# Kernel optimization log

Measured on AMD Instinct MI355X. Metric: run time of the kernel, lower is better.

The kernel has to match this reference:

```python
import jax, jax.numpy as jnp
import numpy as np


def _gru_step(x, h, W_ih, W_hh, b_ih, b_hh):
    # torch GRUCell math, gate order (r, z, n)
    gx = x @ W_ih.T + b_ih
    gh = h @ W_hh.T + b_hh
    xr, xz, xn = jnp.split(gx, 3, axis=-1)
    hr, hz, hn = jnp.split(gh, 3, axis=-1)
    r = jax.nn.sigmoid(xr + hr)
    z = jax.nn.sigmoid(xz + hz)
    n = jnp.tanh(xn + r * hn)
    return (1.0 - z) * n + z * h


def setup_inputs() -> dict:
    T, B, S, E, H, Dv, EXT = 64, 16, 400, 128, 256, 50000, 50
    key = jax.random.key(0)
    ks = jax.random.split(key, 32)
    def rn(k, shape, s=0.05):
        return jax.random.normal(k, shape, dtype=jnp.float32) * s
    return {
        'embedded_y': rn(ks[0], (T, B, E), 1.0),
        'encode_outputs': rn(ks[1], (S, B, 2 * H), 1.0),
        'init_state': rn(ks[2], (B, H), 1.0),
        'x_mask': jnp.ones((S, B, 1), jnp.float32),
        'y_mask': jnp.ones((T, B, 1), jnp.float32),
        'x_index': jax.random.randint(ks[3], (S, B), 0, Dv + EXT),
        'max_ext_len': EXT,
        'init_coverage': jnp.zeros((B, S), jnp.float32),
        'W_h': rn(ks[4], (2 * H, 2 * H)),
        'W_s': rn(ks[5], (2 * H, H)),
        'W_c': rn(ks[6], (2 * H, 1)),
        'b_attn': rn(ks[7], (2 * H,)),
        'V_attn': rn(ks[8], (1, 2 * H)),
        'gru1_Wih': rn(ks[9], (3 * H, E)),
        'gru1_Whh': rn(ks[10], (3 * H, H)),
        'gru1_bih': rn(ks[11], (3 * H,)),
        'gru1_bhh': rn(ks[12], (3 * H,)),
        'gru2_Wih': rn(ks[13], (3 * H, 2 * H)),
        'gru2_Whh': rn(ks[14], (3 * H, H)),
        'gru2_bih': rn(ks[15], (3 * H,)),
        'gru2_bhh': rn(ks[16], (3 * H,)),
        'V1_w': rn(ks[17], (H, H + 2 * H + E)),
        'V1_b': rn(ks[18], (H,)),
        'V2_w': rn(ks[19], (Dv, H)),
        'V2_b': rn(ks[20], (Dv,)),
        'Wp_w': rn(ks[21], (1, H + 2 * H + E)),
        'Wp_b': rn(ks[22], (1,)),
    }


def reference(embedded_y, encode_outputs, init_state, x_mask, y_mask, x_index,
              max_ext_len, init_coverage, W_h, W_s, W_c, b_attn, V_attn,
              gru1_Wih, gru1_Whh, gru1_bih, gru1_bhh,
              gru2_Wih, gru2_Whh, gru2_bih, gru2_bhh,
              V1_w, V1_b, V2_w, V2_b, Wp_w, Wp_b):
    T, B, E = embedded_y.shape
    S = encode_outputs.shape[0]
    enc_proj = encode_outputs @ W_h.T  # [S,B,2H], time-invariant part of attention

    def step(carry, inp):
        hidden, cov = carry  # [B,H], [B,S]
        y_t, ym_t = inp      # [B,E], [B,1]
        s1 = _gru_step(y_t, hidden, gru1_Wih, gru1_Whh, gru1_bih, gru1_bhh)
        s1 = ym_t * s1 + (1.0 - ym_t) * hidden
        # coverage term: cov.T[:,:,None] is [S,B,1], Linear(1,2H)
        att = enc_proj + s1 @ W_s.T + cov.T[:, :, None] @ W_c.T + b_attn  # [S,B,2H]
        score = (jnp.tanh(att) * x_mask) @ V_attn.T                      # [S,B,1]
        score = jnp.where(x_mask == 0, -1e9, score)
        attn = jax.nn.softmax(score, axis=0)                             # over source len
        ctx = jnp.sum(attn * encode_outputs, axis=0)                     # [B,2H]
        s2 = _gru_step(ctx, s1, gru2_Wih, gru2_Whh, gru2_bih, gru2_bhh)
        s2 = ym_t * s2 + (1.0 - ym_t) * s1
        waw = attn[:, :, 0].T                                            # [B,S]
        return (s2, cov + waw), (s2, ctx, waw, cov)

    (_, _), (hs, cvs, waws, covs) = jax.lax.scan(
        step, (init_state, init_coverage), (embedded_y, y_mask))

    # WordProbLayer (pointer-generator)
    h = jnp.concatenate([hs, cvs, embedded_y], axis=2)         # [T,B,H+2H+E]
    logit = jnp.tanh(h @ V1_w.T + V1_b) @ V2_w.T + V2_b        # [T,B,Dv]
    y_dec = jax.nn.softmax(logit, axis=2)
    y_dec = jnp.concatenate(
        [y_dec, jnp.zeros((T, B, max_ext_len), y_dec.dtype)], axis=2)
    g = jax.nn.sigmoid(h @ Wp_w.T + Wp_b)                      # [T,B,1]
    xids = jnp.broadcast_to(x_index.T[None], (T, B, S))        # [T,B,S]
    ti = jnp.arange(T)[:, None, None]
    bi = jnp.arange(B)[None, :, None]
    y_pred = (g * y_dec).at[ti, bi, xids].add((1.0 - g) * waws)
    return (y_pred, hs, waws, covs)
```

## Files before the change

### kernel.cpp

```cpp
#include <hip/hip_runtime.h>
#include <hip/hip_bf16.h>

typedef unsigned short ushort_t;
typedef unsigned int u32;
typedef _Float16 f16;
typedef __attribute__((ext_vector_type(8))) short short8;
typedef __attribute__((ext_vector_type(4))) float f32x4;
typedef __attribute__((ext_vector_type(8))) _Float16 f16x8;
typedef __attribute__((ext_vector_type(4))) unsigned int u32x4;

#define T_ 64
#define B_ 16
#define S_ 400
#define E_ 128
#define H_ 256
#define H2_ 512
#define DV_ 50000
#define VOC_ 50050
#define CAT_ 896
#define NCLUS 8
#define RSL 50

#define YP_SZ   ((size_t)T_*B_*VOC_)
#define HS_OFF  (YP_SZ)
#define WW_OFF  (HS_OFF + (size_t)T_*B_*H_)
#define CV_OFF  (WW_OFF + (size_t)T_*B_*S_)
#define ENCP16_OFF ((size_t)0)
#define ENC16_OFF  ((size_t)1638400)
#define WS16_OFF   ((size_t)3276800)
#define W216_OFF   ((size_t)3342336)
#define CTXALL_OFF ((size_t)3538944)
#define GX1_OFF    ((size_t)4063232)
#define WH216_OFF  ((size_t)4947968)
#define WH116T_OFF ((size_t)5046272)
#define SYNC_OFF   ((size_t)5144576)
#define S1STR      528
#define S1TAG      520
#define S2STR      816
#define S2TAG      808
#define S2REG      ((size_t)16*NCLUS*S1STR)
#define SYNC_FLOATS ((size_t)16*NCLUS*(S1STR + S2STR))
#define WH16F_OFF  ((size_t)5316608)
#define V1HF_OFF   ((size_t)5447680)

#define WS_ROWSUM 0
#define WS_GV     1024
#define WS_G1     2048

__device__ __forceinline__ float fsig(float x){ return 1.f/(1.f+__expf(-x)); }
__device__ __forceinline__ float ftanh(float x){ float e=__expf(2.f*x); return 1.f - 2.f/(e+1.f); }

#define PADK(k) ((k) + (((k)>>5)<<2))

#define AT_ST(p, v)  __hip_atomic_store((p), (v), __ATOMIC_RELAXED, __HIP_MEMORY_SCOPE_AGENT)
#define AT_LD(p)     __hip_atomic_load((p), __ATOMIC_RELAXED, __HIP_MEMORY_SCOPE_AGENT)
#define AT_STI(p, v) __hip_atomic_store((int*)(p), (v), __ATOMIC_RELAXED, __HIP_MEMORY_SCOPE_AGENT)
#define AT_LDI(p)    __hip_atomic_load((const int*)(p), __ATOMIC_RELAXED, __HIP_MEMORY_SCOPE_AGENT)

#define SM_ENC    0
#define SM_ENCP   51200
#define SM_GH1    102400
#define SM_SWS    105472
#define SM_VP     107776
#define SM_WCP    110080
#define SM_UCTX   112384
#define SM_HID    114432
#define SM_S1     115456
#define SM_G2X    116480
#define SM_G2H    116864
#define SM_COV    117248
#define SM_EV     117504
#define SM_XM     117760
#define SM_YM     118016
#define SM_HIDH   118272
#define SM_S1H    118784
#define SM_CTXH   119296
#define SM_S2S    120320
#define SM_PART   120448
#define SM_B1     120512
#define SM_B2     123584
#define SM_B3     126656
#define SM_GX     129728
#define SM_BYTES  132800

__global__ __launch_bounds__(256)
void cvt16_kernel(const float* src, f16* dst, int n){
  int i = blockIdx.x*256 + threadIdx.x;
  if (i < n) dst[i] = (f16)src[i];
}

__global__ __launch_bounds__(256)
void repack_kernel(const float* enc, f16* enc16){
  int s = blockIdx.x, b = blockIdx.y;
  const float* src = enc + ((size_t)s*B_ + b)*H2_;
  f16* dst = enc16 + ((size_t)b*S_ + s)*H2_;
  for (int k = threadIdx.x; k < H2_; k += 256) dst[k] = (f16)src[k];
}

__global__ __launch_bounds__(256)
void packWhh1_kernel(const float* W, f16* dst){
  int r = blockIdx.x, c = threadIdx.x;
  int jq = c >> 5, cc = c & 31;
  dst[((size_t)jq*768 + r)*32 + cc] = (f16)W[(size_t)r*H_ + c];
}

__global__ __launch_bounds__(256)
void gx1_kernel(const float* emb, const float* Wih1, const float* bih1, float* dout){
  __shared__ float As[64][33];
  __shared__ float Bs[128][33];
  int m0 = blockIdx.x*64, n0 = blockIdx.y*128;
  int tx = threadIdx.x & 15, ty = threadIdx.x >> 4;
  float acc[4][8] = {};
  for (int kt = 0; kt < E_; kt += 32){
    for (int l = threadIdx.x; l < 64*32; l += 256){
      int m = l>>5, k = l&31; As[m][k] = emb[(size_t)(m0+m)*E_ + kt + k];
    }
    for (int l = threadIdx.x; l < 128*32; l += 256){
      int n = l>>5, k = l&31; Bs[n][k] = Wih1[(size_t)(n0+n)*E_ + kt + k];
    }
    __syncthreads();
    for (int k = 0; k < 32; ++k){
      float a[4], bv[8];
      #pragma unroll
      for (int i=0;i<4;++i) a[i] = As[ty+16*i][k];
      #pragma unroll
      for (int j=0;j<8;++j) bv[j] = Bs[tx+16*j][k];
      #pragma unroll
      for (int i=0;i<4;++i)
        #pragma unroll
        for (int j=0;j<8;++j) acc[i][j] += a[i]*bv[j];
    }
    __syncthreads();
  }
  #pragma unroll
  for (int i=0;i<4;++i)
    #pragma unroll
    for (int j=0;j<8;++j){
      int m = m0 + ty + 16*i, n = n0 + tx + 16*j;
      dout[GX1_OFF + (size_t)m*768 + n] = acc[i][j] + bih1[n];
    }
}

__global__ __launch_bounds__(256)
void encproj_mfma(const f16* enc16, const f16* Wh16, const float* battn, f16* ep16){
  int nx = blockIdx.x, my = blockIdx.y, bz = blockIdx.z;
  int tid = threadIdx.x;
  int w = tid >> 6, lane = tid & 63;
  int c16 = lane & 15, kg = lane >> 4;
  int m0 = my*64, n0 = nx*128 + w*32;
  f32x4 acc[4][2] = {};
  int col0 = n0 + c16, col1 = n0 + 16 + c16;
  for (int ks = 0; ks < 16; ++ks){
    int k0 = ks*32 + kg*8;
    f16x8 b0 = *(const f16x8*)(Wh16 + (size_t)col0*H2_ + k0);
    f16x8 b1 = *(const f16x8*)(Wh16 + (size_t)col1*H2_ + k0);
    #pragma unroll
    for (int mf = 0; mf < 4; ++mf){
      int s = m0 + mf*16 + c16; if (s > S_-1) s = S_-1;
      f16x8 a = *(const f16x8*)(enc16 + ((size_t)bz*S_ + s)*H2_ + k0);
      acc[mf][0] = __builtin_amdgcn_mfma_f32_16x16x32_f16(a, b0, acc[mf][0], 0, 0, 0);
      acc[mf][1] = __builtin_amdgcn_mfma_f32_16x16x32_f16(a, b1, acc[mf][1], 0, 0, 0);
    }
  }
  #pragma unroll
  for (int mf = 0; mf < 4; ++mf)
    #pragma unroll
    for (int nf = 0; nf < 2; ++nf){
      int col = n0 + nf*16 + c16;
      float bb = battn[col];
      #pragma unroll
      for (int r = 0; r < 4; ++r){
        int s = m0 + mf*16 + kg*4 + r;
        if (s < S_) ep16[((size_t)bz*S_ + s)*H2_ + col] = (f16)(acc[mf][nf][r] + bb);
      }
    }
}

template<int R, int K, bool PAD>
__device__ __forceinline__ void gemv_f16t(const f16* W, const f16* xh, float* out_l, int tid){
  int o = tid >> 3, l8 = tid & 7;
  constexpr int NI = K/64;
  const f16x8* x8 = (const f16x8*)xh;
  f16x8 xv[NI];
  #pragma unroll
  for (int i = 0; i < NI; ++i) xv[i] = x8[i*8 + l8];
  #pragma unroll
  for (int it = 0; it < R/128; ++it){
    int d = o + it*128;
    const f16x8* w8 = (const f16x8*)(W + (size_t)d*K);
    float acc = 0.f;
    #pragma unroll
    for (int i = 0; i < NI; ++i){
      f16x8 w = w8[i*8 + l8];
      #pragma unroll
      for (int e = 0; e < 8; ++e) acc += (float)w[e] * (float)xv[i][e];
    }
    acc += __shfl_xor(acc,1,8); acc += __shfl_xor(acc,2,8); acc += __shfl_xor(acc,4,8);
    if (l8 == 0) out_l[PAD ? PADK(d) : d] = acc;
  }
}

__device__ __forceinline__ void spin_tags(const float* base, int stride, int tagoff, int want, int tid){
  if (tid < 64){
    bool mine = tid < NCLUS;
    const float* tp = base + (size_t)(mine ? tid : 0)*stride + tagoff;
    while (true){
      int v = mine ? AT_LDI(tp) : want;
      if (__all(v == want)) break;
      __builtin_amdgcn_s_sleep(1);
    }
  }
  __syncthreads();
}

__global__ __launch_bounds__(1024)
void scan_kernel(const float* xm, const float* ym,
                 const float* bhh1, const float* bih2, const float* bhh2,
                 const float* Wc, const float* Vat,
                 const float* inith, const float* initc,
                 float* dout)
{
  extern __shared__ char smem[];
  f16*   enc_s  = (f16*)(smem + SM_ENC);
  f16*   encp_s = (f16*)(smem + SM_ENCP);
  float* gh1_l  = (float*)(smem + SM_GH1);
  float* sWs_p  = (float*)(smem + SM_SWS);
  float* Vp     = (float*)(smem + SM_VP);
  float* Wcp    = (float*)(smem + SM_WCP);
  float* uctx   = (float*)(smem + SM_UCTX);
  float* hid_l  = (float*)(smem + SM_HID);
  float* s1_l   = (float*)(smem + SM_S1);
  float* g2x_l  = (float*)(smem + SM_G2X);
  float* g2h_l  = (float*)(smem + SM_G2H);
  float* cov_l  = (float*)(smem + SM_COV);
  float* ev_l   = (float*)(smem + SM_EV);
  float* xm_l   = (float*)(smem + SM_XM);
  float* ym_l   = (float*)(smem + SM_YM);
  f16*   hidh   = (f16*)(smem + SM_HIDH);
  f16*   s1h    = (f16*)(smem + SM_S1H);
  f16*   ctxh   = (f16*)(smem + SM_CTXH);
  float* s2s    = (float*)(smem + SM_S2S);
  float* part_l = (float*)(smem + SM_PART);
  float* b1l    = (float*)(smem + SM_B1);
  float* b2l    = (float*)(smem + SM_B2);
  float* b3l    = (float*)(smem + SM_B3);
  float* gxbuf  = (float*)(smem + SM_GX);

  const f16* Ws16   = (const f16*)(dout + WS16_OFF);
  const f16* W216   = (const f16*)(dout + W216_OFF);
  const f16* Wh216  = (const f16*)(dout + WH216_OFF);
  const f16* Wh116T = (const f16*)(dout + WH116T_OFF);
  const float* gx1  = dout + GX1_OFF;

  int blk = blockIdx.x, tid = threadIdx.x;
  int b = blk & 15, jj = blk >> 4;
  int wv = tid >> 6, ln = tid & 63;

  float* sl1 = dout + SYNC_OFF + (size_t)b*NCLUS*S1STR;
  float* sl2 = dout + SYNC_OFF + S2REG + (size_t)b*NCLUS*S2STR;
  float* sl1my = sl1 + (size_t)jj*S1STR;
  float* sl2my = sl2 + (size_t)jj*S2STR;

  {
    const u32x4* encg  = (const u32x4*)(dout + ENC16_OFF)  + (size_t)b*25600 + jj*3200;
    const u32x4* encpg = (const u32x4*)(dout + ENCP16_OFF) + (size_t)b*25600 + jj*3200;
    u32x4* encs4  = (u32x4*)enc_s;
    u32x4* encps4 = (u32x4*)encp_s;
    for (int i = tid; i < 3200; i += 1024){ encs4[i] = encg[i]; encps4[i] = encpg[i]; }
  }
  if (tid < 32)  s2s[tid] = inith[b*H_ + jj*32 + tid];
  if (tid < 512){ Vp[PADK(tid)] = Vat[tid]; Wcp[PADK(tid)] = Wc[tid]; }
  if (tid < RSL){ int s = jj*RSL + tid; cov_l[tid] = initc[b*S_ + s]; xm_l[tid] = xm[(size_t)s*B_ + b]; }
  if (tid >= 512 && tid < 576) ym_l[tid-512] = ym[(tid-512)*B_ + b];
  if (tid < 768){ b1l[tid] = bhh1[tid]; b2l[tid] = bih2[tid]; b3l[tid] = bhh2[tid];
                  gxbuf[tid] = gx1[(size_t)b*768 + tid]; }
  __syncthreads();
  if (tid < 768){
    const f16x8* p8 = (const f16x8*)(Wh116T + ((size_t)jj*768 + tid)*32);
    float acc = 0.f;
    #pragma unroll
    for (int c4 = 0; c4 < 4; ++c4){
      f16x8 w = p8[c4];
      #pragma unroll
      for (int e = 0; e < 8; ++e) acc += (float)w[e] * s2s[c4*8+e];
    }
    AT_ST(&sl2my[tid], acc);
  } else if (tid < 800){
    AT_ST(&sl2my[768 + (tid-768)], s2s[tid-768]);
  }
  __syncthreads();
  if (tid == 0) AT_STI(&sl2my[S2TAG], 1);

  for (int t = 0; t < T_; ++t){
    int row = t*B_ + b;
    int want = t + 1;
    spin_tags(sl2, S2STR, S2TAG, want, tid);
    if (tid < 768){
      float a = 0.f;
      #pragma unroll
      for (int q = 0; q < NCLUS; ++q) a += AT_LD(&sl2[(size_t)q*S2STR + tid]);
      gh1_l[tid] = a;
    } else {
      int j = tid - 768;
      float h = AT_LD(&sl2[(size_t)(j>>5)*S2STR + 768 + (j&31)]);
      hid_l[j] = h; hidh[j] = (f16)h;
    }
    __syncthreads();
    if (tid < 256){
      int j = tid;
      float r = fsig(gxbuf[j]      + gh1_l[j]      + b1l[j]);
      float z = fsig(gxbuf[256+j]  + gh1_l[256+j]  + b1l[256+j]);
      float n = ftanh(gxbuf[512+j] + r*(gh1_l[512+j] + b1l[512+j]));
      float h = hid_l[j];
      float ymv = ym_l[t];
      float s1 = ymv*((1.f-z)*n + z*h) + (1.f-ymv)*h;
      s1_l[j] = s1; s1h[j] = (f16)s1;
    }
    __syncthreads();
    gemv_f16t<512,256,true>(Ws16, s1h, sWs_p, tid);
    __syncthreads();
    {
      int kp = PADK(ln*8);
      float4 sA = *(const float4*)&sWs_p[kp], sB = *(const float4*)&sWs_p[kp+4];
      float4 vA = *(const float4*)&Vp[kp],    vB = *(const float4*)&Vp[kp+4];
      float4 cA = *(const float4*)&Wcp[kp],   cB = *(const float4*)&Wcp[kp+4];
      const f16x8* eps = (const f16x8*)encp_s;
      #pragma unroll
      for (int i = 0; i < 4; ++i){
        int r = wv + 16*i;
        if (r < RSL){
          f16x8 eu = eps[r*64 + ln];
          float cv = cov_l[r];
          float sc = 0.f;
          sc += ftanh((float)eu[0] + sA.x + cv*cA.x)*vA.x;
          sc += ftanh((float)eu[1] + sA.y + cv*cA.y)*vA.y;
          sc += ftanh((float)eu[2] + sA.z + cv*cA.z)*vA.z;
          sc += ftanh((float)eu[3] + sA.w + cv*cA.w)*vA.w;
          sc += ftanh((float)eu[4] + sB.x + cv*cB.x)*vB.x;
          sc += ftanh((float)eu[5] + sB.y + cv*cB.y)*vB.y;
          sc += ftanh((float)eu[6] + sB.z + cv*cB.z)*vB.z;
          sc += ftanh((float)eu[7] + sB.w + cv*cB.w)*vB.w;
          sc += __shfl_xor(sc,1);  sc += __shfl_xor(sc,2);  sc += __shfl_xor(sc,4);
          sc += __shfl_xor(sc,8);  sc += __shfl_xor(sc,16); sc += __shfl_xor(sc,32);
          if (ln == 0){
            float xmv = xm_l[r];
            ev_l[r] = __expf((xmv == 0.f) ? -1e9f : xmv*sc);
          }
        }
      }
    }
    __syncthreads();
    if (tid < 512){
      float acc = 0.f;
      #pragma unroll 5
      for (int s = 0; s < RSL; ++s) acc += ev_l[s] * (float)enc_s[s*H2_ + tid];
      AT_ST(&sl1my[tid], acc);
    } else if (tid >= 960){
      int l = tid - 960;
      float v = (l < RSL) ? ev_l[l] : 0.f;
      v += __shfl_xor(v,1);  v += __shfl_xor(v,2);  v += __shfl_xor(v,4);
      v += __shfl_xor(v,8);  v += __shfl_xor(v,16); v += __shfl_xor(v,32);
      if (l == 0) AT_ST(&sl1my[512], v);
    }
    __syncthreads();
    if (tid == 0) AT_STI(&sl1my[S1TAG], want);
    float gxn = 0.f;
    if (tid < 768){
      int tn = (t+1 < T_) ? t+1 : t;
      gxn = gx1[(size_t)(tn*B_ + b)*768 + tid];
    }
    {
      int o = tid >> 3, l8 = tid & 7;
      if (o < 96){
        int g = o >> 5, m = o & 31, wrow = g*256 + jj*32 + m;
        const f16x8* w8 = (const f16x8*)(Wh216 + (size_t)wrow*H_);
        const f16x8* x8 = (const f16x8*)s1h;
        float acc = 0.f;
        #pragma unroll
        for (int i = 0; i < 4; ++i){
          f16x8 w = w8[i*8 + l8], x = x8[i*8 + l8];
          #pragma unroll
          for (int e = 0; e < 8; ++e) acc += (float)w[e] * (float)x[e];
        }
        acc += __shfl_xor(acc,1,8); acc += __shfl_xor(acc,2,8); acc += __shfl_xor(acc,4,8);
        if (l8 == 0) g2h_l[o] = acc;
      }
    }
    if (tid < 768) gxbuf[tid] = gxn;
    spin_tags(sl1, S1STR, S1TAG, want, tid);
    if (tid < 512){
      float us = 0.f;
      #pragma unroll
      for (int q = 0; q < NCLUS; ++q) us += AT_LD(&sl1[(size_t)q*S1STR + tid]);
      uctx[tid] = us;
    } else if (tid < 512 + NCLUS){
      part_l[tid-512] = AT_LD(&sl1[(size_t)(tid-512)*S1STR + 512]);
    }
    __syncthreads();
    {
      float es = 0.f;
      #pragma unroll
      for (int q = 0; q < NCLUS; ++q) es += part_l[q];
      float inv = 1.f/es;
      if (tid < 512){
        float v = uctx[tid]*inv;
        ctxh[tid] = (f16)v;
        if (jj == 0) __builtin_nontemporal_store(v, &dout[CTXALL_OFF + (size_t)row*H2_ + tid]);
      } else if (tid >= 640 && tid < 640 + RSL){
        int r = tid - 640;
        float w_ = ev_l[r]*inv;
        size_t ro = (size_t)row*S_ + jj*RSL + r;
        __builtin_nontemporal_store(w_, &dout[WW_OFF + ro]);
        float co = cov_l[r];
        __builtin_nontemporal_store(co, &dout[CV_OFF + ro]);
        cov_l[r] = co + w_;
      }
    }
    __syncthreads();
    {
      int o = tid >> 3, l8 = tid & 7;
      if (o < 96){
        int g = o >> 5, m = o & 31, wrow = g*256 + jj*32 + m;
        const f16x8* w8 = (const f16x8*)(W216 + (size_t)wrow*H2_);
        const f16x8* x8 = (const f16x8*)ctxh;
        float acc = 0.f;
        #pragma unroll
        for (int i = 0; i < 8; ++i){
          f16x8 w = w8[i*8 + l8], x = x8[i*8 + l8];
          #pragma unroll
          for (int e = 0; e < 8; ++e) acc += (float)w[e] * (float)x[e];
        }
        acc += __shfl_xor(acc,1,8); acc += __shfl_xor(acc,2,8); acc += __shfl_xor(acc,4,8);
        if (l8 == 0) g2x_l[o] = acc;
      }
    }
    __syncthreads();
    if (tid < 32){
      int i = tid, j = jj*32 + i;
      float r = fsig(g2x_l[i]     + b2l[j]     + g2h_l[i]    + b3l[j]);
      float z = fsig(g2x_l[32+i]  + b2l[256+j] + g2h_l[32+i] + b3l[256+j]);
      float n = ftanh(g2x_l[64+i] + b2l[512+j] + r*(g2h_l[64+i] + b3l[512+j]));
      float s1v = s1_l[j];
      float ymv = ym_l[t];
      float s2 = ymv*((1.f-z)*n + z*s1v) + (1.f-ymv)*s1v;
      s2s[i] = s2;
      AT_ST(&sl2my[768 + i], s2);
      __builtin_nontemporal_store(s2, &dout[HS_OFF + (size_t)row*H_ + j]);
    }
    __syncthreads();
    if (tid < 768){
      const f16x8* p8 = (const f16x8*)(Wh116T + ((size_t)jj*768 + tid)*32);
      float acc = 0.f;
      #pragma unroll
      for (int c4 = 0; c4 < 4; ++c4){
        f16x8 w = p8[c4];
        #pragma unroll
        for (int e = 0; e < 8; ++e) acc += (float)w[e] * s2s[c4*8+e];
      }
      AT_ST(&sl2my[tid], acc);
    }
    __syncthreads();
    if (tid == 0) AT_STI(&sl2my[S2TAG], t + 2);
  }
}

__global__ __launch_bounds__(512)
void head_kernel(const float* emb, const f16* V1H, const float* V1b,
                 const float* Wpw, const float* Wpb, float* dout, float* ws)
{
  __shared__ float hc[2][CAT_];
  int t = blockIdx.x, b0 = blockIdx.y*2, tid = threadIdx.x;
  for (int i = tid; i < 2*CAT_; i += 512){
    int bb = i / CAT_, k = i % CAT_;
    int b = b0 + bb;
    float v;
    if (k < H_)           v = dout[HS_OFF     + ((size_t)(t*B_+b))*H_  + k];
    else if (k < H_+H2_)  v = dout[CTXALL_OFF + ((size_t)(t*B_+b))*H2_ + (k-H_)];
    else                  v = emb[((size_t)(t*B_+b))*E_ + (k-H_-H2_)];
    hc[bb][k] = v;
  }
  __syncthreads();
  __hip_bfloat16* G1 = (__hip_bfloat16*)(ws + WS_G1);
  {
    int j = tid & 255, bb = tid >> 8;
    const f16x8* wv8 = (const f16x8*)(V1H + (size_t)j*CAT_);
    float acc = 0.f;
    #pragma unroll 4
    for (int kk = 0; kk < CAT_/8; ++kk){
      f16x8 w = wv8[kk];
      #pragma unroll
      for (int e = 0; e < 8; ++e) acc += hc[bb][kk*8+e]*(float)w[e];
    }
    G1[((size_t)(t*B_ + b0 + bb))*H_ + j] = __float2bfloat16(ftanh(acc + V1b[j]));
  }
  if (tid < 128){
    int bb = tid >> 6, l = tid & 63;
    float acc = 0.f;
    for (int k = l; k < CAT_; k += 64) acc += hc[bb][k]*Wpw[k];
    acc += __shfl_xor(acc,1);  acc += __shfl_xor(acc,2);  acc += __shfl_xor(acc,4);
    acc += __shfl_xor(acc,8);  acc += __shfl_xor(acc,16); acc += __shfl_xor(acc,32);
    if (l == 0) ws[WS_GV + t*B_ + b0 + bb] = fsig(acc + Wpb[0]);
  }
}

__global__ __launch_bounds__(256)
void gemm2_kernel(const ushort_t* G1, const float* V2w, const float* V2b,
                  float* dout, float* rowsum)
{
  __shared__ float rows_l[128];
  int tid = threadIdx.x;
  if (tid < 128) rows_l[tid] = 0.f;
  int m0 = blockIdx.y * 128;
  int n0 = blockIdx.x * 64;
  int lane = tid & 63, w = tid >> 6;
  int c16 = lane & 15, kg = lane >> 4;
  int col = n0 + w*16 + c16;
  int colc = col < DV_ ? col : DV_-1;
  bool valid = col < DV_;
  f32x4 acc[8] = {};
  const float* brow = V2w + (size_t)colc*H_;
  for (int ks = 0; ks < 8; ++ks){
    int k0 = ks*32 + kg*8;
    short8 bf;
    #pragma unroll
    for (int i = 0; i < 8; ++i){
      __hip_bfloat16 hb = __float2bfloat16(brow[k0+i]);
      union { __hip_bfloat16 h; short s; } u; u.h = hb;
      bf[i] = u.s;
    }
    #pragma unroll
    for (int mf = 0; mf < 8; ++mf){
      const short8* ap = (const short8*)(G1 + ((size_t)(m0 + mf*16 + c16))*H_ + k0);
      acc[mf] = __builtin_amdgcn_mfma_f32_16x16x32_bf16(*ap, bf, acc[mf], 0, 0, 0);
    }
  }
  float bias = valid ? V2b[colc] : 0.f;
  __syncthreads();
  #pragma unroll
  for (int mf = 0; mf < 8; ++mf){
    #pragma unroll
    for (int r = 0; r < 4; ++r){
      float v = valid ? __expf(acc[mf][r] + bias) : 0.f;
      int rloc = mf*16 + kg*4 + r;
      if (valid) dout[(size_t)(m0 + rloc)*VOC_ + col] = v;
      float s = v;
      s += __shfl_xor(s, 1, 16); s += __shfl_xor(s, 2, 16);
      s += __shfl_xor(s, 4, 16); s += __shfl_xor(s, 8, 16);
      if (c16 == 0) atomicAdd(&rows_l[rloc], s);
    }
  }
  __syncthreads();
  if (tid < 128) atomicAdd(&rowsum[m0 + tid], rows_l[tid]);
}

__global__ __launch_bounds__(256)
void normscatter_kernel(float* dout, const float* ws, const int* xidx){
  int row = blockIdx.x; int b = row & 15;
  float gv = ws[WS_GV + row];
  float sc = gv / ws[WS_ROWSUM + row];
  float g1 = 1.f - gv;
  float2* y2 = (float2*)(dout + (size_t)row * VOC_);
  for (int i = threadIdx.x; i < VOC_/2; i += 256){
    float2 v = y2[i];
    int e0 = 2*i;
    v.x = (e0   < DV_) ? v.x*sc : 0.f;
    v.y = (e0+1 < DV_) ? v.y*sc : 0.f;
    y2[i] = v;
  }
  __syncthreads();
  const float* ww = dout + WW_OFF + (size_t)row*S_;
  float* y = dout + (size_t)row*VOC_;
  for (int s = threadIdx.x; s < S_; s += 256){
    atomicAdd(&y[xidx[(size_t)s*B_ + b]], g1*ww[s]);
  }
}

extern "C" void kernel_launch(void* const* d_in, const int* in_sizes, int n_in,
                              void* d_out, int out_size, void* d_ws, size_t ws_size,
                              hipStream_t stream)
{
  (void)in_sizes; (void)n_in; (void)out_size; (void)ws_size;
  const float* emb   = (const float*)d_in[0];
  const float* enc   = (const float*)d_in[1];
  const float* inith = (const float*)d_in[2];
  const float* xmask = (const float*)d_in[3];
  const float* ymask = (const float*)d_in[4];
  const int*   xidx  = (const int*)d_in[5];
  const float* initc = (const float*)d_in[7];
  const float* Wh    = (const float*)d_in[8];
  const float* Wss   = (const float*)d_in[9];
  const float* Wc    = (const float*)d_in[10];
  const float* battn = (const float*)d_in[11];
  const float* Vat   = (const float*)d_in[12];
  const float* Wih1  = (const float*)d_in[13];
  const float* Whh1  = (const float*)d_in[14];
  const float* bih1  = (const float*)d_in[15];
  const float* bhh1  = (const float*)d_in[16];
  const float* Wih2  = (const float*)d_in[17];
  const float* Whh2  = (const float*)d_in[18];
  const float* bih2  = (const float*)d_in[19];
  const float* bhh2  = (const float*)d_in[20];
  const float* V1w   = (const float*)d_in[21];
  const float* V1b   = (const float*)d_in[22];
  const float* V2w   = (const float*)d_in[23];
  const float* V2b   = (const float*)d_in[24];
  const float* Wpw   = (const float*)d_in[25];
  const float* Wpb   = (const float*)d_in[26];
  float* out = (float*)d_out;
  float* ws  = (float*)d_ws;

  hipFuncSetAttribute(reinterpret_cast<const void*>(scan_kernel),
                      hipFuncAttributeMaxDynamicSharedMemorySize, SM_BYTES);

  hipMemsetAsync(d_ws, 0, 2048*sizeof(float), stream);
  hipMemsetAsync(out + SYNC_OFF, 0, SYNC_FLOATS*sizeof(float), stream);
  cvt16_kernel<<<512,  256, 0, stream>>>(Wss,  (f16*)(out + WS16_OFF), H2_*H_);
  cvt16_kernel<<<1536, 256, 0, stream>>>(Wih2, (f16*)(out + W216_OFF), 3*H_*H2_);
  cvt16_kernel<<<768,  256, 0, stream>>>(Whh2, (f16*)(out + WH216_OFF), 3*H_*H_);
  cvt16_kernel<<<1024, 256, 0, stream>>>(Wh,   (f16*)(out + WH16F_OFF), H2_*H2_);
  cvt16_kernel<<<896,  256, 0, stream>>>(V1w,  (f16*)(out + V1HF_OFF), H_*CAT_);
  packWhh1_kernel<<<768, 256, 0, stream>>>(Whh1, (f16*)(out + WH116T_OFF));
  repack_kernel<<<dim3(S_, B_), 256, 0, stream>>>(enc, (f16*)(out + ENC16_OFF));
  gx1_kernel<<<dim3(16, 6), 256, 0, stream>>>(emb, Wih1, bih1, out);
  encproj_mfma<<<dim3(4, 7, B_), 256, 0, stream>>>((const f16*)(out + ENC16_OFF),
      (const f16*)(out + WH16F_OFF), battn, (f16*)(out + ENCP16_OFF));
  scan_kernel<<<128, 1024, SM_BYTES, stream>>>(xmask, ymask,
      bhh1, bih2, bhh2, Wc, Vat, inith, initc, out);
  head_kernel<<<dim3(T_, 8), 512, 0, stream>>>(emb, (const f16*)(out + V1HF_OFF),
      V1b, Wpw, Wpb, out, ws);
  gemm2_kernel<<<dim3(782, 8), 256, 0, stream>>>((const ushort_t*)(ws + WS_G1), V2w, V2b, out, ws + WS_ROWSUM);
  normscatter_kernel<<<1024, 256, 0, stream>>>(out, ws, xidx);
}
```

Measured before the change: 1.888 ms.

## Remove scan-step barriers by fusing reductions and doubling gemm2 row tile

```diff
diff --git a/kernel.cpp b/kernel.cpp
--- a/kernel.cpp
+++ b/kernel.cpp
@@ -63,20 +63,15 @@
 #define SM_SWS    105472
 #define SM_VP     107776
 #define SM_WCP    110080
-#define SM_UCTX   112384
-#define SM_HID    114432
 #define SM_S1     115456
-#define SM_G2X    116480
 #define SM_G2H    116864
 #define SM_COV    117248
 #define SM_EV     117504
 #define SM_XM     117760
 #define SM_YM     118016
-#define SM_HIDH   118272
 #define SM_S1H    118784
 #define SM_CTXH   119296
 #define SM_S2S    120320
-#define SM_PART   120448
 #define SM_B1     120512
 #define SM_B2     123584
 #define SM_B3     126656
@@ -223,24 +218,18 @@
   extern __shared__ char smem[];
   f16*   enc_s  = (f16*)(smem + SM_ENC);
   f16*   encp_s = (f16*)(smem + SM_ENCP);
-  float* gh1_l  = (float*)(smem + SM_GH1);
   float* sWs_p  = (float*)(smem + SM_SWS);
   float* Vp     = (float*)(smem + SM_VP);
   float* Wcp    = (float*)(smem + SM_WCP);
-  float* uctx   = (float*)(smem + SM_UCTX);
-  float* hid_l  = (float*)(smem + SM_HID);
   float* s1_l   = (float*)(smem + SM_S1);
-  float* g2x_l  = (float*)(smem + SM_G2X);
   float* g2h_l  = (float*)(smem + SM_G2H);
   float* cov_l  = (float*)(smem + SM_COV);
   float* ev_l   = (float*)(smem + SM_EV);
   float* xm_l   = (float*)(smem + SM_XM);
   float* ym_l   = (float*)(smem + SM_YM);
-  f16*   hidh   = (f16*)(smem + SM_HIDH);
   f16*   s1h    = (f16*)(smem + SM_S1H);
   f16*   ctxh   = (f16*)(smem + SM_CTXH);
   float* s2s    = (float*)(smem + SM_S2S);
-  float* part_l = (float*)(smem + SM_PART);
   float* b1l    = (float*)(smem + SM_B1);
   float* b2l    = (float*)(smem + SM_B2);
   float* b3l    = (float*)(smem + SM_B3);
@@ -295,23 +284,18 @@
     int row = t*B_ + b;
     int want = t + 1;
     spin_tags(sl2, S2STR, S2TAG, want, tid);
-    if (tid < 768){
-      float a = 0.f;
-      #pragma unroll
-      for (int q = 0; q < NCLUS; ++q) a += AT_LD(&sl2[(size_t)q*S2STR + tid]);
-      gh1_l[tid] = a;
-    } else {
-      int j = tid - 768;
-      float h = AT_LD(&sl2[(size_t)(j>>5)*S2STR + 768 + (j&31)]);
-      hid_l[j] = h; hidh[j] = (f16)h;
-    }
-    __syncthreads();
     if (tid < 256){
       int j = tid;
-      float r = fsig(gxbuf[j]      + gh1_l[j]      + b1l[j]);
-      float z = fsig(gxbuf[256+j]  + gh1_l[256+j]  + b1l[256+j]);
-      float n = ftanh(gxbuf[512+j] + r*(gh1_l[512+j] + b1l[512+j]));
-      float h = hid_l[j];
+      float ar = 0.f, az = 0.f, an = 0.f;
+      #pragma unroll
+      for (int q = 0; q < NCLUS; ++q){
+        const float* sq = sl2 + (size_t)q*S2STR;
+        ar += AT_LD(&sq[j]); az += AT_LD(&sq[256+j]); an += AT_LD(&sq[512+j]);
+      }
+      float h = AT_LD(&sl2[(size_t)(j>>5)*S2STR + 768 + (j&31)]);
+      float r = fsig(gxbuf[j]      + ar + b1l[j]);
+      float z = fsig(gxbuf[256+j]  + az + b1l[256+j]);
+      float n = ftanh(gxbuf[512+j] + r*(an + b1l[512+j]));
       float ymv = ym_l[t];
       float s1 = ymv*((1.f-z)*n + z*h) + (1.f-ymv)*h;
       s1_l[j] = s1; s1h[j] = (f16)s1;
@@ -371,39 +355,43 @@
     }
     {
       int o = tid >> 3, l8 = tid & 7;
-      if (o < 96){
-        int g = o >> 5, m = o & 31, wrow = g*256 + jj*32 + m;
-        const f16x8* w8 = (const f16x8*)(Wh216 + (size_t)wrow*H_);
-        const f16x8* x8 = (const f16x8*)s1h;
-        float acc = 0.f;
+      if (o < 32){
+        int j = jj*32 + o;
+        const f16x8* y8 = (const f16x8*)s1h;
+        f16x8 ya[4];
+        #pragma unroll
+        for (int i = 0; i < 4; ++i) ya[i] = y8[i*8 + l8];
+        float ar = 0.f, az = 0.f, an = 0.f;
+        const f16x8* wr = (const f16x8*)(Wh216 + (size_t)j*H_);
+        const f16x8* wz = (const f16x8*)(Wh216 + (size_t)(256+j)*H_);
+        const f16x8* wn = (const f16x8*)(Wh216 + (size_t)(512+j)*H_);
         #pragma unroll
         for (int i = 0; i < 4; ++i){
-          f16x8 w = w8[i*8 + l8], x = x8[i*8 + l8];
+          f16x8 a = wr[i*8 + l8], c = wz[i*8 + l8], d = wn[i*8 + l8];
           #pragma unroll
-          for (int e = 0; e < 8; ++e) acc += (float)w[e] * (float)x[e];
+          for (int e = 0; e < 8; ++e){
+            float xv = (float)ya[i][e];
+            ar += (float)a[e]*xv; az += (float)c[e]*xv; an += (float)d[e]*xv;
+          }
         }
-        acc += __shfl_xor(acc,1,8); acc += __shfl_xor(acc,2,8); acc += __shfl_xor(acc,4,8);
-        if (l8 == 0) g2h_l[o] = acc;
+        ar += __shfl_xor(ar,1,8); ar += __shfl_xor(ar,2,8); ar += __shfl_xor(ar,4,8);
+        az += __shfl_xor(az,1,8); az += __shfl_xor(az,2,8); az += __shfl_xor(az,4,8);
+        an += __shfl_xor(an,1,8); an += __shfl_xor(an,2,8); an += __shfl_xor(an,4,8);
+        if (l8 == 0){ g2h_l[o] = ar; g2h_l[32+o] = az; g2h_l[64+o] = an; }
       }
     }
     if (tid < 768) gxbuf[tid] = gxn;
     spin_tags(sl1, S1STR, S1TAG, want, tid);
-    if (tid < 512){
-      float us = 0.f;
-      #pragma unroll
-      for (int q = 0; q < NCLUS; ++q) us += AT_LD(&sl1[(size_t)q*S1STR + tid]);
-      uctx[tid] = us;
-    } else if (tid < 512 + NCLUS){
-      part_l[tid-512] = AT_LD(&sl1[(size_t)(tid-512)*S1STR + 512]);
-    }
-    __syncthreads();
     {
       float es = 0.f;
       #pragma unroll
-      for (int q = 0; q < NCLUS; ++q) es += part_l[q];
+      for (int q = 0; q < NCLUS; ++q) es += AT_LD(&sl1[(size_t)q*S1STR + 512]);
       float inv = 1.f/es;
       if (tid < 512){
-        float v = uctx[tid]*inv;
+        float us = 0.f;
+        #pragma unroll
+        for (int q = 0; q < NCLUS; ++q) us += AT_LD(&sl1[(size_t)q*S1STR + tid]);
+        float v = us*inv;
         ctxh[tid] = (f16)v;
         if (jj == 0) __builtin_nontemporal_store(v, &dout[CTXALL_OFF + (size_t)row*H2_ + tid]);
       } else if (tid >= 640 && tid < 640 + RSL){
@@ -419,33 +407,40 @@
     __syncthreads();
     {
       int o = tid >> 3, l8 = tid & 7;
-      if (o < 96){
-        int g = o >> 5, m = o & 31, wrow = g*256 + jj*32 + m;
-        const f16x8* w8 = (const f16x8*)(W216 + (size_t)wrow*H2_);
+      if (o < 32){
+        int j = jj*32 + o;
         const f16x8* x8 = (const f16x8*)ctxh;
-        float acc = 0.f;
+        f16x8 xa[8];
+        #pragma unroll
+        for (int i = 0; i < 8; ++i) xa[i] = x8[i*8 + l8];
+        float ar = 0.f, az = 0.f, an = 0.f;
+        const f16x8* wr = (const f16x8*)(W216 + (size_t)j*H2_);
+        const f16x8* wz = (const f16x8*)(W216 + (size_t)(256+j)*H2_);
+        const f16x8* wn = (const f16x8*)(W216 + (size_t)(512+j)*H2_);
         #pragma unroll
         for (int i = 0; i < 8; ++i){
-          f16x8 w = w8[i*8 + l8], x = x8[i*8 + l8];
+          f16x8 a = wr[i*8 + l8], c = wz[i*8 + l8], d = wn[i*8 + l8];
           #pragma unroll
-          for (int e = 0; e < 8; ++e) acc += (float)w[e] * (float)x[e];
+          for (int e = 0; e < 8; ++e){
+            float xv = (float)xa[i][e];
+            ar += (float)a[e]*xv; az += (float)c[e]*xv; an += (float)d[e]*xv;
+          }
         }
-        acc += __shfl_xor(acc,1,8); acc += __shfl_xor(acc,2,8); acc += __shfl_xor(acc,4,8);
-        if (l8 == 0) g2x_l[o] = acc;
+        ar += __shfl_xor(ar,1,8); ar += __shfl_xor(ar,2,8); ar += __shfl_xor(ar,4,8);
+        az += __shfl_xor(az,1,8); az += __shfl_xor(az,2,8); az += __shfl_xor(az,4,8);
+        an += __shfl_xor(an,1,8); an += __shfl_xor(an,2,8); an += __shfl_xor(an,4,8);
+        if (l8 == 0){
+          float gr = fsig(ar + b2l[j]     + g2h_l[o]    + b3l[j]);
+          float gz = fsig(az + b2l[256+j] + g2h_l[32+o] + b3l[256+j]);
+          float gn = ftanh(an + b2l[512+j] + gr*(g2h_l[64+o] + b3l[512+j]));
+          float s1v = s1_l[j];
+          float ymv = ym_l[t];
+          float s2 = ymv*((1.f-gz)*gn + gz*s1v) + (1.f-ymv)*s1v;
+          s2s[o] = s2;
+          AT_ST(&sl2my[768 + o], s2);
+          __builtin_nontemporal_store(s2, &dout[HS_OFF + (size_t)row*H_ + j]);
+        }
       }
-    }
-    __syncthreads();
-    if (tid < 32){
-      int i = tid, j = jj*32 + i;
-      float r = fsig(g2x_l[i]     + b2l[j]     + g2h_l[i]    + b3l[j]);
-      float z = fsig(g2x_l[32+i]  + b2l[256+j] + g2h_l[32+i] + b3l[256+j]);
-      float n = ftanh(g2x_l[64+i] + b2l[512+j] + r*(g2h_l[64+i] + b3l[512+j]));
-      float s1v = s1_l[j];
-      float ymv = ym_l[t];
-      float s2 = ymv*((1.f-z)*n + z*s1v) + (1.f-ymv)*s1v;
-      s2s[i] = s2;
-      AT_ST(&sl2my[768 + i], s2);
-      __builtin_nontemporal_store(s2, &dout[HS_OFF + (size_t)row*H_ + j]);
     }
     __syncthreads();
     if (tid < 768){
@@ -507,17 +502,17 @@
 void gemm2_kernel(const ushort_t* G1, const float* V2w, const float* V2b,
                   float* dout, float* rowsum)
 {
-  __shared__ float rows_l[128];
+  __shared__ float rows_l[256];
   int tid = threadIdx.x;
-  if (tid < 128) rows_l[tid] = 0.f;
-  int m0 = blockIdx.y * 128;
+  rows_l[tid] = 0.f;
+  int m0 = blockIdx.y * 256;
   int n0 = blockIdx.x * 64;
   int lane = tid & 63, w = tid >> 6;
   int c16 = lane & 15, kg = lane >> 4;
   int col = n0 + w*16 + c16;
   int colc = col < DV_ ? col : DV_-1;
   bool valid = col < DV_;
-  f32x4 acc[8] = {};
+  f32x4 acc[16] = {};
   const float* brow = V2w + (size_t)colc*H_;
   for (int ks = 0; ks < 8; ++ks){
     int k0 = ks*32 + kg*8;
@@ -529,7 +524,7 @@
       bf[i] = u.s;
     }
     #pragma unroll
-    for (int mf = 0; mf < 8; ++mf){
+    for (int mf = 0; mf < 16; ++mf){
       const short8* ap = (const short8*)(G1 + ((size_t)(m0 + mf*16 + c16))*H_ + k0);
       acc[mf] = __builtin_amdgcn_mfma_f32_16x16x32_bf16(*ap, bf, acc[mf], 0, 0, 0);
     }
@@ -537,12 +532,12 @@
   float bias = valid ? V2b[colc] : 0.f;
   __syncthreads();
   #pragma unroll
-  for (int mf = 0; mf < 8; ++mf){
+  for (int mf = 0; mf < 16; ++mf){
     #pragma unroll
     for (int r = 0; r < 4; ++r){
       float v = valid ? __expf(acc[mf][r] + bias) : 0.f;
       int rloc = mf*16 + kg*4 + r;
-      if (valid) dout[(size_t)(m0 + rloc)*VOC_ + col] = v;
+      if (valid) __builtin_nontemporal_store(v, &dout[(size_t)(m0 + rloc)*VOC_ + col]);
       float s = v;
       s += __shfl_xor(s, 1, 16); s += __shfl_xor(s, 2, 16);
       s += __shfl_xor(s, 4, 16); s += __shfl_xor(s, 8, 16);
@@ -550,7 +545,7 @@
     }
   }
   __syncthreads();
-  if (tid < 128) atomicAdd(&rowsum[m0 + tid], rows_l[tid]);
+  atomicAdd(&rowsum[m0 + tid], rows_l[tid]);
 }
 
 __global__ __launch_bounds__(256)
@@ -628,6 +623,6 @@
       bhh1, bih2, bhh2, Wc, Vat, inith, initc, out);
   head_kernel<<<dim3(T_, 8), 512, 0, stream>>>(emb, (const f16*)(out + V1HF_OFF),
       V1b, Wpw, Wpb, out, ws);
-  gemm2_kernel<<<dim3(782, 8), 256, 0, stream>>>((const ushort_t*)(ws + WS_G1), V2w, V2b, out, ws + WS_ROWSUM);
+  gemm2_kernel<<<dim3(782, 4), 256, 0, stream>>>((const ushort_t*)(ws + WS_G1), V2w, V2b, out, ws + WS_ROWSUM);
   normscatter_kernel<<<1024, 256, 0, stream>>>(out, ws, xidx);
 }
```

New measurement: 2.411 ms. 27.7% more time.
